# Kernel tuning notes

Measured on AMD Instinct MI355X. Metric: run time of the kernel, lower is better.

## Reference

```python
import jax, jax.numpy as jnp
import numpy as np
from jax import lax

MAX_LENGTH = 10
SOS_TOKEN = 0
B, S, H, V = 64, 128, 1024, 32000


def setup_inputs() -> dict:
    key = jax.random.key(0)
    ks = jax.random.split(key, 16)
    sc = 0.02
    return {
        "encoder_outputs": jax.random.normal(ks[0], (B, S, H), jnp.float32),
        "hidden": jax.random.normal(ks[1], (1, B, H), jnp.float32),
        "target": jax.random.randint(ks[2], (B, MAX_LENGTH), 0, V, jnp.int32),
        "emb_W": jax.random.normal(ks[3], (V, H), jnp.float32) * sc,
        "Wa_w": jax.random.normal(ks[4], (H, H), jnp.float32) * sc,
        "Wa_b": jnp.zeros((H,), jnp.float32),
        "Ua_w": jax.random.normal(ks[5], (H, H), jnp.float32) * sc,
        "Ua_b": jnp.zeros((H,), jnp.float32),
        "Va_w": jax.random.normal(ks[6], (1, H), jnp.float32) * sc,
        "Va_b": jnp.zeros((1,), jnp.float32),
        "W_ih": jax.random.normal(ks[7], (3 * H, 2 * H), jnp.float32) * sc,
        "W_hh": jax.random.normal(ks[8], (3 * H, H), jnp.float32) * sc,
        "b_ih": jnp.zeros((3 * H,), jnp.float32),
        "b_hh": jnp.zeros((3 * H,), jnp.float32),
        "out_W": jax.random.normal(ks[9], (V, H), jnp.float32) * sc,
        "out_b": jnp.zeros((V,), jnp.float32),
    }


def reference(encoder_outputs, hidden, target, emb_W, Wa_w, Wa_b, Ua_w, Ua_b,
              Va_w, Va_b, W_ih, W_hh, b_ih, b_hh, out_W, out_b):
    # teacher-forced decoder input tokens: [SOS, target[:, :T-1]]
    sos = jnp.full((target.shape[0], 1), SOS_TOKEN, target.dtype)
    tokens = jnp.concatenate([sos, target[:, :MAX_LENGTH - 1]], axis=1)  # [B,T]

    # Ua(keys) is constant across steps -> hoist (same math as per-step recompute)
    Uk = jnp.einsum('bsh,gh->bsg', encoder_outputs, Ua_w) + Ua_b  # [B,S,H]

    def step(h, tok):  # h: [B,H], tok: [B]
        emb = emb_W[tok]                                   # [B,H]
        q = h @ Wa_w.T + Wa_b                              # [B,H]
        score = jnp.tanh(q[:, None, :] + Uk) @ Va_w[0] + Va_b[0]  # [B,S]
        w = jax.nn.softmax(score, axis=-1)                 # [B,S]
        ctx = jnp.einsum('bs,bsh->bh', w, encoder_outputs) # [B,H]
        x = jnp.concatenate([emb, ctx], axis=-1)           # [B,2H]
        gi = x @ W_ih.T + b_ih
        gh = h @ W_hh.T + b_hh
        ir, iz, inn = jnp.split(gi, 3, axis=-1)
        hr, hz, hn = jnp.split(gh, 3, axis=-1)
        r = jax.nn.sigmoid(ir + hr)
        z = jax.nn.sigmoid(iz + hz)
        n = jnp.tanh(inn + r * hn)
        h_new = (1.0 - z) * n + z * h
        logits = h_new @ out_W.T + out_b                   # [B,V]
        return h_new, (logits, w)

    hT, (outs, ws) = lax.scan(step, hidden[0], tokens.T)   # outs [T,B,V]
    outputs = jnp.transpose(outs, (1, 0, 2))               # [B,T,V]
    attns = jnp.transpose(ws, (1, 0, 2))                   # [B,T,S]
    return jax.nn.log_softmax(outputs, axis=-1), hT[None], attns
```

## Files before the change

kernel.cpp:

```cpp
#include <hip/hip_runtime.h>

#define B_  64
#define S_  128
#define H_  1024
#define V_  32000
#define T_  10

typedef unsigned short ushort_t;
typedef unsigned int uint32;
typedef __attribute__((ext_vector_type(8))) short bf16x8;
typedef __attribute__((ext_vector_type(4))) float f32x4;

__device__ __forceinline__ ushort_t f2bf(float x) {
    uint32 u = __float_as_uint(x);
    u += 0x7fffu + ((u >> 16) & 1u);
    return (ushort_t)(u >> 16);
}
__device__ __forceinline__ float bf2f(ushort_t h) {
    return __uint_as_float(((uint32)h) << 16);
}
__device__ __forceinline__ uint32 pk2(float a, float b) {
    return (uint32)f2bf(a) | ((uint32)f2bf(b) << 16);
}

typedef const __attribute__((address_space(1))) void gas_void;
typedef __attribute__((address_space(3))) void las_void;
__device__ __forceinline__ void gload_lds16(const ushort_t* g, ushort_t* l) {
    __builtin_amdgcn_global_load_lds((gas_void*)g, (las_void*)l, 16, 0, 0);
}

template<int BM, int BN, int WC, bool SPLIT, bool AF32, int CMODE>
__launch_bounds__(256)
__global__ void gemm_bf(const float* __restrict__ Af,
                        const ushort_t* __restrict__ Ah, const ushort_t* __restrict__ Al,
                        int lda,
                        const ushort_t* __restrict__ Bh, const ushort_t* __restrict__ Bl,
                        int ldb,
                        int K, int kchunk,
                        const float* __restrict__ bias,
                        float* __restrict__ C, int ldc, size_t czstride)
{
    constexpr int WR = 4 / WC;
    constexpr int MF = BM / WR / 16;
    constexpr int NF = BN / WC / 16;
    __shared__ __align__(16) ushort_t lds[(SPLIT ? 2 : 1) * (BM + BN) * 32];
    ushort_t* ldsAh = lds;
    ushort_t* ldsAl = lds + BM * 32;
    ushort_t* ldsBh = lds + (SPLIT ? 2 : 1) * BM * 32;
    ushort_t* ldsBl = ldsBh + BN * 32;

    const int tid  = threadIdx.x;
    const int wid  = tid >> 6;
    const int lane = tid & 63;
    const int lr   = lane & 15;
    const int lk   = lane >> 4;
    const int m0   = blockIdx.y * BM;
    const int n0   = blockIdx.x * BN;
    const int wrow = wid / WC, wcol = wid % WC;
    const int mW   = wrow * (BM / WR);
    const int nW   = wcol * (BN / WC);

    f32x4 acc[MF][NF];
    #pragma unroll
    for (int i = 0; i < MF; i++)
        #pragma unroll
        for (int j = 0; j < NF; j++)
            acc[i][j] = (f32x4){0.f, 0.f, 0.f, 0.f};

    const int kbeg = blockIdx.z * kchunk;
    const int kend = (kbeg + kchunk < K) ? (kbeg + kchunk) : K;

    for (int k0 = kbeg; k0 < kend; k0 += 32) {
        __syncthreads();
        if constexpr (AF32) {
            #pragma unroll
            for (int p = 0; p < BM * 4 / 256; p++) {
                int c = p * 256 + tid, row = c >> 2, slot = c & 3;
                const float* src = Af + (size_t)(m0 + row) * lda + k0 + slot * 8;
                float4 x0 = *(const float4*)src;
                float4 x1 = *(const float4*)(src + 4);
                uint4 hv;
                hv.x = pk2(x0.x, x0.y); hv.y = pk2(x0.z, x0.w);
                hv.z = pk2(x1.x, x1.y); hv.w = pk2(x1.z, x1.w);
                *(uint4*)&ldsAh[row * 32 + slot * 8] = hv;
                if constexpr (SPLIT) {
                    uint4 lv;
                    lv.x = pk2(x0.x - bf2f((ushort_t)(hv.x & 0xffff)), x0.y - bf2f((ushort_t)(hv.x >> 16)));
                    lv.y = pk2(x0.z - bf2f((ushort_t)(hv.y & 0xffff)), x0.w - bf2f((ushort_t)(hv.y >> 16)));
                    lv.z = pk2(x1.x - bf2f((ushort_t)(hv.z & 0xffff)), x1.y - bf2f((ushort_t)(hv.z >> 16)));
                    lv.w = pk2(x1.z - bf2f((ushort_t)(hv.w & 0xffff)), x1.w - bf2f((ushort_t)(hv.w >> 16)));
                    *(uint4*)&ldsAl[row * 32 + slot * 8] = lv;
                }
            }
        } else {
            for (int is = wid; is < BM / 16; is += 4) {
                int row = is * 16 + (lane >> 2), chk = lane & 3;
                size_t off = (size_t)(m0 + row) * lda + k0 + chk * 8;
                gload_lds16(Ah + off, &ldsAh[is * 512]);
                if constexpr (SPLIT) gload_lds16(Al + off, &ldsAl[is * 512]);
            }
        }
        for (int is = wid; is < BN / 16; is += 4) {
            int row = is * 16 + (lane >> 2), chk = lane & 3;
            size_t off = (size_t)(n0 + row) * ldb + k0 + chk * 8;
            gload_lds16(Bh + off, &ldsBh[is * 512]);
            if constexpr (SPLIT) gload_lds16(Bl + off, &ldsBl[is * 512]);
        }
        __syncthreads();
        bf16x8 aH[MF], bH[NF], aL[MF], bL[NF];
        #pragma unroll
        for (int i = 0; i < MF; i++) {
            aH[i] = *(const bf16x8*)&ldsAh[(mW + i * 16 + lr) * 32 + lk * 8];
            if constexpr (SPLIT) aL[i] = *(const bf16x8*)&ldsAl[(mW + i * 16 + lr) * 32 + lk * 8];
        }
        #pragma unroll
        for (int j = 0; j < NF; j++) {
            bH[j] = *(const bf16x8*)&ldsBh[(nW + j * 16 + lr) * 32 + lk * 8];
            if constexpr (SPLIT) bL[j] = *(const bf16x8*)&ldsBl[(nW + j * 16 + lr) * 32 + lk * 8];
        }
        #pragma unroll
        for (int i = 0; i < MF; i++)
            #pragma unroll
            for (int j = 0; j < NF; j++) {
                acc[i][j] = __builtin_amdgcn_mfma_f32_16x16x32_bf16(aH[i], bH[j], acc[i][j], 0, 0, 0);
                if constexpr (SPLIT) {
                    acc[i][j] = __builtin_amdgcn_mfma_f32_16x16x32_bf16(aH[i], bL[j], acc[i][j], 0, 0, 0);
                    acc[i][j] = __builtin_amdgcn_mfma_f32_16x16x32_bf16(aL[i], bH[j], acc[i][j], 0, 0, 0);
                }
            }
    }
    float* Cz = C + (size_t)blockIdx.z * czstride;
    #pragma unroll
    for (int i = 0; i < MF; i++)
        #pragma unroll
        for (int j = 0; j < NF; j++)
            #pragma unroll
            for (int r = 0; r < 4; r++) {
                int gr  = m0 + mW + i * 16 + lk * 4 + r;
                int col = n0 + nW + j * 16 + lr;
                float v = acc[i][j][r];
                if (CMODE == 0) {
                    if (bias) v += bias[col];
                    Cz[(size_t)gr * ldc + col] = v;
                } else {
                    int b = gr & 63, t = gr >> 6;
                    C[((size_t)(b * T_ + t)) * V_ + col] = v + bias[col];
                }
            }
}

__global__ __launch_bounds__(256) void cast_bf16_k(const float* __restrict__ in,
                                                   ushort_t* __restrict__ out, int n8)
{
    int i = blockIdx.x * 256 + threadIdx.x;
    if (i < n8) {
        float4 a = ((const float4*)in)[2 * i];
        float4 b = ((const float4*)in)[2 * i + 1];
        uint4 v;
        v.x = pk2(a.x, a.y); v.y = pk2(a.z, a.w);
        v.z = pk2(b.x, b.y); v.w = pk2(b.z, b.w);
        ((uint4*)out)[i] = v;
    }
}

__global__ __launch_bounds__(256) void cast_hilo_k(const float* __restrict__ in,
                                                   ushort_t* __restrict__ hi,
                                                   ushort_t* __restrict__ lo, int n8)
{
    int i = blockIdx.x * 256 + threadIdx.x;
    if (i < n8) {
        float4 a = ((const float4*)in)[2 * i];
        float4 b = ((const float4*)in)[2 * i + 1];
        uint4 hv, lv;
        hv.x = pk2(a.x, a.y); hv.y = pk2(a.z, a.w);
        hv.z = pk2(b.x, b.y); hv.w = pk2(b.z, b.w);
        lv.x = pk2(a.x - bf2f((ushort_t)(hv.x & 0xffff)), a.y - bf2f((ushort_t)(hv.x >> 16)));
        lv.y = pk2(a.z - bf2f((ushort_t)(hv.y & 0xffff)), a.w - bf2f((ushort_t)(hv.y >> 16)));
        lv.z = pk2(b.x - bf2f((ushort_t)(hv.z & 0xffff)), b.y - bf2f((ushort_t)(hv.z >> 16)));
        lv.w = pk2(b.z - bf2f((ushort_t)(hv.w & 0xffff)), b.w - bf2f((ushort_t)(hv.w >> 16)));
        ((uint4*)hi)[i] = hv;
        ((uint4*)lo)[i] = lv;
    }
}

__global__ __launch_bounds__(256) void gatherhl_k(const int* __restrict__ target,
                                                  const float* __restrict__ emb_W,
                                                  ushort_t* __restrict__ Eh,
                                                  ushort_t* __restrict__ El)
{
    int idx = blockIdx.x * 256 + threadIdx.x;
    int r = idx >> 7, c8 = idx & 127;
    int t = r >> 6, b = r & 63;
    int tok = (t == 0) ? 0 : target[b * T_ + t - 1];
    const float* src = emb_W + (size_t)tok * H_ + c8 * 8;
    float4 a = *(const float4*)src;
    float4 c = *(const float4*)(src + 4);
    uint4 hv, lv;
    hv.x = pk2(a.x, a.y); hv.y = pk2(a.z, a.w);
    hv.z = pk2(c.x, c.y); hv.w = pk2(c.z, c.w);
    lv.x = pk2(a.x - bf2f((ushort_t)(hv.x & 0xffff)), a.y - bf2f((ushort_t)(hv.x >> 16)));
    lv.y = pk2(a.z - bf2f((ushort_t)(hv.y & 0xffff)), a.w - bf2f((ushort_t)(hv.y >> 16)));
    lv.z = pk2(c.x - bf2f((ushort_t)(hv.z & 0xffff)), c.y - bf2f((ushort_t)(hv.z >> 16)));
    lv.w = pk2(c.z - bf2f((ushort_t)(hv.w & 0xffff)), c.w - bf2f((ushort_t)(hv.w >> 16)));
    ((uint4*)(Eh + (size_t)r * H_))[c8] = hv;
    ((uint4*)(El + (size_t)r * H_))[c8] = lv;
}

__global__ __launch_bounds__(256) void score_k(const float* __restrict__ Uk,
                                               const float* __restrict__ qgh_part,
                                               const float* __restrict__ Wa_b,
                                               const float* __restrict__ Va_w,
                                               const float* __restrict__ Va_b,
                                               float* __restrict__ scores)
{
    int s = blockIdx.x, b = blockIdx.y;
    int tid = threadIdx.x;
    float4 qq = ((const float4*)Wa_b)[tid];
    #pragma unroll
    for (int kz = 0; kz < 4; kz++) {
        float4 p = ((const float4*)(qgh_part + (size_t)kz * B_ * 4096 + (size_t)b * 4096))[tid];
        qq.x += p.x; qq.y += p.y; qq.z += p.z; qq.w += p.w;
    }
    float4 u = ((const float4*)(Uk + ((size_t)b * S_ + s) * H_))[tid];
    float4 v = ((const float4*)Va_w)[tid];
    float acc = v.x * tanhf(u.x + qq.x) + v.y * tanhf(u.y + qq.y)
              + v.z * tanhf(u.z + qq.z) + v.w * tanhf(u.w + qq.w);
    for (int off = 32; off > 0; off >>= 1) acc += __shfl_down(acc, off, 64);
    __shared__ float part[4];
    if ((tid & 63) == 0) part[tid >> 6] = acc;
    __syncthreads();
    if (tid == 0) scores[b * S_ + s] = part[0] + part[1] + part[2] + part[3] + Va_b[0];
}

__global__ __launch_bounds__(256) void softctx_k(const float* __restrict__ scores,
                                                 const float* __restrict__ enc,
                                                 ushort_t* __restrict__ ctx_hi,
                                                 ushort_t* __restrict__ ctx_lo,
                                                 float* __restrict__ attn_out, int t)
{
    int hc = blockIdx.x, b = blockIdx.y;
    int tid = threadIdx.x;
    __shared__ float sc[S_], el[S_];
    if (tid < S_) sc[tid] = scores[b * S_ + tid];
    __syncthreads();
    float mx = -1e30f;
    for (int s = 0; s < S_; s++) mx = fmaxf(mx, sc[s]);
    if (tid < S_) el[tid] = expf(sc[tid] - mx);
    __syncthreads();
    float sum = 0.f;
    for (int s = 0; s < S_; s++) sum += el[s];
    float inv = 1.f / sum;
    int h = hc * 256 + tid;
    const float* ep = enc + (size_t)b * S_ * H_ + h;
    float acc = 0.f;
    for (int s = 0; s < S_; s++) acc += el[s] * ep[(size_t)s * H_];
    acc *= inv;
    ushort_t chi = f2bf(acc);
    ctx_hi[(size_t)b * H_ + h] = chi;
    ctx_lo[(size_t)b * H_ + h] = f2bf(acc - bf2f(chi));
    if (hc == 0 && tid < S_) attn_out[((size_t)b * T_ + t) * S_ + tid] = el[tid] * inv;
}

__global__ __launch_bounds__(256) void combine_k(const float* __restrict__ giemb_t,
                                                 const float* __restrict__ gi_part,
                                                 const float* __restrict__ qgh_part,
                                                 const ushort_t* __restrict__ Hh,
                                                 const ushort_t* __restrict__ Hl,
                                                 int t,
                                                 float* __restrict__ out_hidden,
                                                 const float* __restrict__ b_hh)
{
    int i = blockIdx.x * 256 + threadIdx.x;
    int b = i >> 10, g = i & 1023;
    float ir = giemb_t[(size_t)b * 3072 + g];
    float iz = giemb_t[(size_t)b * 3072 + 1024 + g];
    float in = giemb_t[(size_t)b * 3072 + 2048 + g];
    float hr = b_hh[g], hz = b_hh[1024 + g], hn_ = b_hh[2048 + g];
    #pragma unroll
    for (int kz = 0; kz < 4; kz++) {
        const float* gp = gi_part + (size_t)kz * B_ * 3072 + (size_t)b * 3072;
        ir += gp[g]; iz += gp[1024 + g]; in += gp[2048 + g];
        const float* qp = qgh_part + (size_t)kz * B_ * 4096 + (size_t)b * 4096 + 1024;
        hr += qp[g]; hz += qp[1024 + g]; hn_ += qp[2048 + g];
    }
    float h = bf2f(Hh[(size_t)t * B_ * H_ + i]) + bf2f(Hl[(size_t)t * B_ * H_ + i]);
    float r = 1.f / (1.f + expf(-(ir + hr)));
    float z = 1.f / (1.f + expf(-(iz + hz)));
    float n = tanhf(in + r * hn_);
    float hn = (1.f - z) * n + z * h;
    ushort_t hih = f2bf(hn);
    ushort_t* Hhw = (ushort_t*)Hh; ushort_t* Hlw = (ushort_t*)Hl;
    Hhw[(size_t)(t + 1) * B_ * H_ + i] = hih;
    Hlw[(size_t)(t + 1) * B_ * H_ + i] = f2bf(hn - bf2f(hih));
    if (out_hidden) out_hidden[i] = hn;
}

__global__ __launch_bounds__(1024) void lsm_k(float* __restrict__ out)
{
    float4* p = (float4*)(out + (size_t)blockIdx.x * V_);
    int tid = threadIdx.x;
    float mx = -1e30f, sm = 0.f;
    for (int v = tid; v < V_ / 4; v += 1024) {
        float4 x = p[v];
        float xs[4] = {x.x, x.y, x.z, x.w};
        #pragma unroll
        for (int j = 0; j < 4; j++) {
            float m2 = fmaxf(mx, xs[j]);
            sm = sm * expf(mx - m2) + expf(xs[j] - m2);
            mx = m2;
        }
    }
    for (int off = 32; off > 0; off >>= 1) {
        float mo = __shfl_down(mx, off, 64);
        float so = __shfl_down(sm, off, 64);
        float m2 = fmaxf(mx, mo);
        sm = sm * expf(mx - m2) + so * expf(mo - m2);
        mx = m2;
    }
    __shared__ float pm[16], ps[16];
    __shared__ float lse_s;
    if ((tid & 63) == 0) { pm[tid >> 6] = mx; ps[tid >> 6] = sm; }
    __syncthreads();
    if (tid == 0) {
        float m = pm[0], s = ps[0];
        for (int i = 1; i < 16; i++) {
            float m2 = fmaxf(m, pm[i]);
            s = s * expf(m - m2) + ps[i] * expf(pm[i] - m2);
            m = m2;
        }
        lse_s = m + logf(s);
    }
    __syncthreads();
    float lse = lse_s;
    for (int v = tid; v < V_ / 4; v += 1024) {
        float4 x = p[v];
        x.x -= lse; x.y -= lse; x.z -= lse; x.w -= lse;
        p[v] = x;
    }
}

extern "C" void kernel_launch(void* const* d_in, const int* in_sizes, int n_in,
                              void* d_out, int out_size, void* d_ws, size_t ws_size,
                              hipStream_t stream)
{
    (void)in_sizes; (void)n_in; (void)out_size; (void)ws_size;
    const float* enc    = (const float*)d_in[0];
    const float* hidden = (const float*)d_in[1];
    const int*   target = (const int*)d_in[2];
    const float* emb_W  = (const float*)d_in[3];
    const float* Wa_w   = (const float*)d_in[4];
    const float* Wa_b   = (const float*)d_in[5];
    const float* Ua_w   = (const float*)d_in[6];
    const float* Ua_b   = (const float*)d_in[7];
    const float* Va_w   = (const float*)d_in[8];
    const float* Va_b   = (const float*)d_in[9];
    const float* W_ih   = (const float*)d_in[10];
    const float* W_hh   = (const float*)d_in[11];
    const float* b_ih   = (const float*)d_in[12];
    const float* b_hh   = (const float*)d_in[13];
    const float* out_W  = (const float*)d_in[14];
    const float* out_b  = (const float*)d_in[15];

    float* out_logits = (float*)d_out;
    float* out_hidden = out_logits + (size_t)B_ * T_ * V_;
    float* out_attn   = out_hidden + (size_t)B_ * H_;

    char* w = (char*)d_ws;
    auto alloc = [&](size_t bytes) { char* p = w; w += (bytes + 255) & ~(size_t)255; return p; };
    ushort_t* outW_bf = (ushort_t*)alloc((size_t)V_ * H_ * 2);
    float*    Uk      = (float*)alloc((size_t)B_ * S_ * H_ * 4);
    ushort_t* Ua_hi   = (ushort_t*)alloc((size_t)H_ * H_ * 2);
    ushort_t* Ua_lo   = (ushort_t*)alloc((size_t)H_ * H_ * 2);
    ushort_t* Wih_hi  = (ushort_t*)alloc((size_t)3 * H_ * 2 * H_ * 2);
    ushort_t* Wih_lo  = (ushort_t*)alloc((size_t)3 * H_ * 2 * H_ * 2);
    ushort_t* Wc_hi   = (ushort_t*)alloc((size_t)4 * H_ * H_ * 2);
    ushort_t* Wc_lo   = (ushort_t*)alloc((size_t)4 * H_ * H_ * 2);
    ushort_t* E_hi    = (ushort_t*)alloc((size_t)T_ * B_ * H_ * 2);
    ushort_t* E_lo    = (ushort_t*)alloc((size_t)T_ * B_ * H_ * 2);
    ushort_t* H_hi    = (ushort_t*)alloc((size_t)(T_ + 1) * B_ * H_ * 2);
    ushort_t* H_lo    = (ushort_t*)alloc((size_t)(T_ + 1) * B_ * H_ * 2);
    float*    giemb   = (float*)alloc((size_t)T_ * B_ * 3 * H_ * 4);
    float*    gi_part = (float*)alloc((size_t)4 * B_ * 3 * H_ * 4);
    float*    qgh_part= (float*)alloc((size_t)4 * B_ * 4 * H_ * 4);
    ushort_t* ctx_hi  = (ushort_t*)alloc((size_t)B_ * H_ * 2);
    ushort_t* ctx_lo  = (ushort_t*)alloc((size_t)B_ * H_ * 2);
    float*    scores  = (float*)alloc((size_t)B_ * S_ * 4);

    cast_bf16_k<<<V_ * H_ / 8 / 256, 256, 0, stream>>>(out_W, outW_bf, V_ * H_ / 8);
    cast_hilo_k<<<H_ * H_ / 8 / 256, 256, 0, stream>>>(Ua_w, Ua_hi, Ua_lo, H_ * H_ / 8);
    cast_hilo_k<<<3 * H_ * 2 * H_ / 8 / 256, 256, 0, stream>>>(W_ih, Wih_hi, Wih_lo, 3 * H_ * 2 * H_ / 8);
    cast_hilo_k<<<H_ * H_ / 8 / 256, 256, 0, stream>>>(Wa_w, Wc_hi, Wc_lo, H_ * H_ / 8);
    cast_hilo_k<<<3 * H_ * H_ / 8 / 256, 256, 0, stream>>>(W_hh, Wc_hi + (size_t)H_ * H_,
                                                           Wc_lo + (size_t)H_ * H_, 3 * H_ * H_ / 8);
    cast_hilo_k<<<B_ * H_ / 8 / 256, 256, 0, stream>>>(hidden, H_hi, H_lo, B_ * H_ / 8);
    gatherhl_k<<<T_ * B_ * H_ / 8 / 256, 256, 0, stream>>>(target, emb_W, E_hi, E_lo);

    gemm_bf<128, 128, 2, true, true, 0><<<dim3(H_ / 128, B_ * S_ / 128, 1), 256, 0, stream>>>(
        enc, nullptr, nullptr, H_, Ua_hi, Ua_lo, H_, H_, H_, Ua_b, Uk, H_, 0);
    gemm_bf<128, 128, 2, true, false, 0><<<dim3(3 * H_ / 128, T_ * B_ / 128, 1), 256, 0, stream>>>(
        nullptr, E_hi, E_lo, H_, Wih_hi, Wih_lo, 2 * H_, H_, H_, b_ih, giemb, 3 * H_, 0);

    for (int t = 0; t < T_; t++) {
        float* gi_t = giemb + (size_t)t * B_ * 3 * H_;
        const ushort_t* hh = H_hi + (size_t)t * B_ * H_;
        const ushort_t* hl = H_lo + (size_t)t * B_ * H_;
        gemm_bf<64, 64, 4, true, false, 0><<<dim3(4 * H_ / 64, 1, 4), 256, 0, stream>>>(
            nullptr, hh, hl, H_, Wc_hi, Wc_lo, H_, H_, H_ / 4, nullptr,
            qgh_part, 4 * H_, (size_t)B_ * 4 * H_);
        score_k<<<dim3(S_, B_), 256, 0, stream>>>(Uk, qgh_part, Wa_b, Va_w, Va_b, scores);
        softctx_k<<<dim3(H_ / 256, B_), 256, 0, stream>>>(scores, enc, ctx_hi, ctx_lo, out_attn, t);
        gemm_bf<64, 64, 4, true, false, 0><<<dim3(3 * H_ / 64, 1, 4), 256, 0, stream>>>(
            nullptr, ctx_hi, ctx_lo, H_, Wih_hi + H_, Wih_lo + H_, 2 * H_, H_, H_ / 4, nullptr,
            gi_part, 3 * H_, (size_t)B_ * 3 * H_);
        combine_k<<<B_ * H_ / 256, 256, 0, stream>>>(
            gi_t, gi_part, qgh_part, H_hi, H_lo, t,
            (t == T_ - 1) ? out_hidden : nullptr, b_hh);
    }

    gemm_bf<128, 128, 2, false, false, 2><<<dim3(V_ / 128, T_ * B_ / 128, 1), 256, 0, stream>>>(
        nullptr, H_hi + (size_t)B_ * H_, nullptr, H_, outW_bf, nullptr, H_, H_, H_,
        out_b, out_logits, 0, 0);
    lsm_k<<<B_ * T_, 1024, 0, stream>>>(out_logits);
}
```

Baseline: 988.9 us.

## Fuse ctx-GEMM with GRU combine, batch casts, add XCD-aware tile swizzle

Replaces the split-K context GEMM plus separate combine kernel with a single gigru_k that computes the context part of the input gates and applies the GRU update in its epilogue. This removes the gi_part partial buffer and one launch per step. All hi/lo casts, including the encoder outputs, are merged into one grid-stride kernel, so the Uk GEMM now loads pre-split bf16 instead of converting fp32 in its inner loop. An XCD-aware block-index swizzle is added to the large GEMMs to improve L2 locality. The trade-offs are that gigru_k runs only 32 blocks with a full K loop, and the encoder cast adds a pass over memory.

```diff
diff --git a/kernel.cpp b/kernel.cpp
--- a/kernel.cpp
+++ b/kernel.cpp
@@ -29,16 +29,16 @@
     __builtin_amdgcn_global_load_lds((gas_void*)g, (las_void*)l, 16, 0, 0);
 }
 
-template<int BM, int BN, int WC, bool SPLIT, bool AF32, int CMODE>
+template<int BM, int BN, int WC, bool SPLIT, int CMODE, int SWZ>
 __launch_bounds__(256)
-__global__ void gemm_bf(const float* __restrict__ Af,
-                        const ushort_t* __restrict__ Ah, const ushort_t* __restrict__ Al,
+__global__ void gemm_bf(const ushort_t* __restrict__ Ah, const ushort_t* __restrict__ Al,
                         int lda,
                         const ushort_t* __restrict__ Bh, const ushort_t* __restrict__ Bl,
                         int ldb,
                         int K, int kchunk,
                         const float* __restrict__ bias,
-                        float* __restrict__ C, int ldc, size_t czstride)
+                        float* __restrict__ C, int ldc, size_t czstride,
+                        int swz_q, int swz_r)
 {
     constexpr int WR = 4 / WC;
     constexpr int MF = BM / WR / 16;
@@ -54,8 +54,21 @@
     const int lane = tid & 63;
     const int lr   = lane & 15;
     const int lk   = lane >> 4;
-    const int m0   = blockIdx.y * BM;
-    const int n0   = blockIdx.x * BN;
+
+    int m_i, n_i;
+    if (SWZ == 0) {
+        m_i = blockIdx.y; n_i = blockIdx.x;
+    } else {
+        int lin = blockIdx.y * gridDim.x + blockIdx.x;
+        int xcd = lin & 7, idx = lin >> 3;
+        int w = (xcd < swz_r) ? xcd * (swz_q + 1) + idx
+                              : swz_r * (swz_q + 1) + (xcd - swz_r) * swz_q + idx;
+        if (SWZ == 1) { m_i = w / (int)gridDim.x; n_i = w % (int)gridDim.x; }
+        else          { m_i = w % (int)gridDim.y; n_i = w / (int)gridDim.y; }
+    }
+    const int m0 = m_i * BM;
+    const int n0 = n_i * BN;
+
     const int wrow = wid / WC, wcol = wid % WC;
     const int mW   = wrow * (BM / WR);
     const int nW   = wcol * (BN / WC);
@@ -72,33 +85,11 @@
 
     for (int k0 = kbeg; k0 < kend; k0 += 32) {
         __syncthreads();
-        if constexpr (AF32) {
-            #pragma unroll
-            for (int p = 0; p < BM * 4 / 256; p++) {
-                int c = p * 256 + tid, row = c >> 2, slot = c & 3;
-                const float* src = Af + (size_t)(m0 + row) * lda + k0 + slot * 8;
-                float4 x0 = *(const float4*)src;
-                float4 x1 = *(const float4*)(src + 4);
-                uint4 hv;
-                hv.x = pk2(x0.x, x0.y); hv.y = pk2(x0.z, x0.w);
-                hv.z = pk2(x1.x, x1.y); hv.w = pk2(x1.z, x1.w);
-                *(uint4*)&ldsAh[row * 32 + slot * 8] = hv;
-                if constexpr (SPLIT) {
-                    uint4 lv;
-                    lv.x = pk2(x0.x - bf2f((ushort_t)(hv.x & 0xffff)), x0.y - bf2f((ushort_t)(hv.x >> 16)));
-                    lv.y = pk2(x0.z - bf2f((ushort_t)(hv.y & 0xffff)), x0.w - bf2f((ushort_t)(hv.y >> 16)));
-                    lv.z = pk2(x1.x - bf2f((ushort_t)(hv.z & 0xffff)), x1.y - bf2f((ushort_t)(hv.z >> 16)));
-                    lv.w = pk2(x1.z - bf2f((ushort_t)(hv.w & 0xffff)), x1.w - bf2f((ushort_t)(hv.w >> 16)));
-                    *(uint4*)&ldsAl[row * 32 + slot * 8] = lv;
-                }
-            }
-        } else {
-            for (int is = wid; is < BM / 16; is += 4) {
-                int row = is * 16 + (lane >> 2), chk = lane & 3;
-                size_t off = (size_t)(m0 + row) * lda + k0 + chk * 8;
-                gload_lds16(Ah + off, &ldsAh[is * 512]);
-                if constexpr (SPLIT) gload_lds16(Al + off, &ldsAl[is * 512]);
-            }
+        for (int is = wid; is < BM / 16; is += 4) {
+            int row = is * 16 + (lane >> 2), chk = lane & 3;
+            size_t off = (size_t)(m0 + row) * lda + k0 + chk * 8;
+            gload_lds16(Ah + off, &ldsAh[is * 512]);
+            if constexpr (SPLIT) gload_lds16(Al + off, &ldsAl[is * 512]);
         }
         for (int is = wid; is < BN / 16; is += 4) {
             int row = is * 16 + (lane >> 2), chk = lane & 3;
@@ -149,6 +140,108 @@
             }
 }
 
+__launch_bounds__(256)
+__global__ void gigru_k(const ushort_t* __restrict__ ctx_hi, const ushort_t* __restrict__ ctx_lo,
+                        const ushort_t* __restrict__ W2h, const ushort_t* __restrict__ W2l,
+                        const float* __restrict__ giemb_t,
+                        const float* __restrict__ qgh_part,
+                        const float* __restrict__ b_hh,
+                        ushort_t* __restrict__ Hh, ushort_t* __restrict__ Hl,
+                        int t, float* __restrict__ out_hidden)
+{
+    constexpr int BM = 64, BN = 96;
+    __shared__ __align__(16) ushort_t lds[(BM + BN) * 32 * 2];
+    __shared__ float gi_lds[64][97];
+    ushort_t* ldsAh = lds;
+    ushort_t* ldsAl = lds + BM * 32;
+    ushort_t* ldsBh = lds + 2 * BM * 32;
+    ushort_t* ldsBl = ldsBh + BN * 32;
+
+    const int tid = threadIdx.x, wid = tid >> 6, lane = tid & 63;
+    const int lr = lane & 15, lk = lane >> 4;
+    const int g0 = blockIdx.x * 32;
+    const int wr = wid >> 1, wc = wid & 1;
+    const int mW = wr * 32, nW = wc * 48;
+
+    f32x4 acc[2][3];
+    #pragma unroll
+    for (int i = 0; i < 2; i++)
+        #pragma unroll
+        for (int j = 0; j < 3; j++)
+            acc[i][j] = (f32x4){0.f, 0.f, 0.f, 0.f};
+
+    for (int k0 = 0; k0 < H_; k0 += 32) {
+        __syncthreads();
+        {
+            int row = wid * 16 + (lane >> 2);
+            size_t off = (size_t)row * H_ + k0 + (lane & 3) * 8;
+            gload_lds16(ctx_hi + off, &ldsAh[wid * 512]);
+            gload_lds16(ctx_lo + off, &ldsAl[wid * 512]);
+        }
+        for (int is = wid; is < 6; is += 4) {
+            int br = is * 16 + (lane >> 2);
+            int grow = (br >> 5) * H_ + g0 + (br & 31);
+            size_t off = (size_t)grow * (2 * H_) + k0 + (lane & 3) * 8;
+            gload_lds16(W2h + off, &ldsBh[is * 512]);
+            gload_lds16(W2l + off, &ldsBl[is * 512]);
+        }
+        __syncthreads();
+        bf16x8 aH[2], aL[2], bH[3], bL[3];
+        #pragma unroll
+        for (int i = 0; i < 2; i++) {
+            aH[i] = *(const bf16x8*)&ldsAh[(mW + i * 16 + lr) * 32 + lk * 8];
+            aL[i] = *(const bf16x8*)&ldsAl[(mW + i * 16 + lr) * 32 + lk * 8];
+        }
+        #pragma unroll
+        for (int j = 0; j < 3; j++) {
+            bH[j] = *(const bf16x8*)&ldsBh[(nW + j * 16 + lr) * 32 + lk * 8];
+            bL[j] = *(const bf16x8*)&ldsBl[(nW + j * 16 + lr) * 32 + lk * 8];
+        }
+        #pragma unroll
+        for (int i = 0; i < 2; i++)
+            #pragma unroll
+            for (int j = 0; j < 3; j++) {
+                acc[i][j] = __builtin_amdgcn_mfma_f32_16x16x32_bf16(aH[i], bH[j], acc[i][j], 0, 0, 0);
+                acc[i][j] = __builtin_amdgcn_mfma_f32_16x16x32_bf16(aH[i], bL[j], acc[i][j], 0, 0, 0);
+                acc[i][j] = __builtin_amdgcn_mfma_f32_16x16x32_bf16(aL[i], bH[j], acc[i][j], 0, 0, 0);
+            }
+    }
+    __syncthreads();
+    #pragma unroll
+    for (int i = 0; i < 2; i++)
+        #pragma unroll
+        for (int j = 0; j < 3; j++)
+            #pragma unroll
+            for (int r = 0; r < 4; r++)
+                gi_lds[mW + i * 16 + lk * 4 + r][nW + j * 16 + lr] = acc[i][j][r];
+    __syncthreads();
+    #pragma unroll
+    for (int kk = 0; kk < 8; kk++) {
+        int c = kk * 256 + tid;
+        int gl = c & 31, b = c >> 5;
+        int g = g0 + gl;
+        float ir = giemb_t[(size_t)b * 3072 + g]        + gi_lds[b][gl];
+        float iz = giemb_t[(size_t)b * 3072 + 1024 + g] + gi_lds[b][32 + gl];
+        float in = giemb_t[(size_t)b * 3072 + 2048 + g] + gi_lds[b][64 + gl];
+        float hr = b_hh[g], hz = b_hh[1024 + g], hn_ = b_hh[2048 + g];
+        #pragma unroll
+        for (int kz = 0; kz < 4; kz++) {
+            const float* qp = qgh_part + (size_t)kz * B_ * 4096 + (size_t)b * 4096 + 1024;
+            hr += qp[g]; hz += qp[1024 + g]; hn_ += qp[2048 + g];
+        }
+        size_t ih = (size_t)t * B_ * H_ + (size_t)b * H_ + g;
+        float h = bf2f(Hh[ih]) + bf2f(Hl[ih]);
+        float r = 1.f / (1.f + expf(-(ir + hr)));
+        float z = 1.f / (1.f + expf(-(iz + hz)));
+        float n = tanhf(in + r * hn_);
+        float hn = (1.f - z) * n + z * h;
+        ushort_t hih = f2bf(hn);
+        Hh[ih + B_ * H_] = hih;
+        Hl[ih + B_ * H_] = f2bf(hn - bf2f(hih));
+        if (out_hidden) out_hidden[(size_t)b * H_ + g] = hn;
+    }
+}
+
 __global__ __launch_bounds__(256) void cast_bf16_k(const float* __restrict__ in,
                                                    ushort_t* __restrict__ out, int n8)
 {
@@ -163,14 +256,37 @@
     }
 }
 
-__global__ __launch_bounds__(256) void cast_hilo_k(const float* __restrict__ in,
-                                                   ushort_t* __restrict__ hi,
-                                                   ushort_t* __restrict__ lo, int n8)
-{
-    int i = blockIdx.x * 256 + threadIdx.x;
-    if (i < n8) {
-        float4 a = ((const float4*)in)[2 * i];
-        float4 b = ((const float4*)in)[2 * i + 1];
+#define CAN0 1048576
+#define CAN1 131072
+#define CAN2 786432
+#define CAN3 131072
+#define CAN4 393216
+#define CAN5 8192
+#define CAC1 (CAN0)
+#define CAC2 (CAC1+CAN1)
+#define CAC3 (CAC2+CAN2)
+#define CAC4 (CAC3+CAN3)
+#define CAC5 (CAC4+CAN4)
+#define CATOT (CAC5+CAN5)
+__global__ __launch_bounds__(256) void castall_k(const float* __restrict__ s0,
+                                                 const float* __restrict__ s1,
+                                                 const float* __restrict__ s2,
+                                                 const float* __restrict__ s3,
+                                                 const float* __restrict__ s4,
+                                                 const float* __restrict__ s5,
+                                                 ushort_t* __restrict__ hi,
+                                                 ushort_t* __restrict__ lo)
+{
+    for (int i = blockIdx.x * 256 + threadIdx.x; i < CATOT; i += gridDim.x * 256) {
+        const float* s; int j;
+        if      (i < CAC1) { s = s0; j = i; }
+        else if (i < CAC2) { s = s1; j = i - CAC1; }
+        else if (i < CAC3) { s = s2; j = i - CAC2; }
+        else if (i < CAC4) { s = s3; j = i - CAC3; }
+        else if (i < CAC5) { s = s4; j = i - CAC4; }
+        else               { s = s5; j = i - CAC5; }
+        float4 a = ((const float4*)s)[2 * j];
+        float4 b = ((const float4*)s)[2 * j + 1];
         uint4 hv, lv;
         hv.x = pk2(a.x, a.y); hv.y = pk2(a.z, a.w);
         hv.z = pk2(b.x, b.y); hv.w = pk2(b.z, b.w);
@@ -259,40 +375,6 @@
     ctx_hi[(size_t)b * H_ + h] = chi;
     ctx_lo[(size_t)b * H_ + h] = f2bf(acc - bf2f(chi));
     if (hc == 0 && tid < S_) attn_out[((size_t)b * T_ + t) * S_ + tid] = el[tid] * inv;
-}
-
-__global__ __launch_bounds__(256) void combine_k(const float* __restrict__ giemb_t,
-                                                 const float* __restrict__ gi_part,
-                                                 const float* __restrict__ qgh_part,
-                                                 const ushort_t* __restrict__ Hh,
-                                                 const ushort_t* __restrict__ Hl,
-                                                 int t,
-                                                 float* __restrict__ out_hidden,
-                                                 const float* __restrict__ b_hh)
-{
-    int i = blockIdx.x * 256 + threadIdx.x;
-    int b = i >> 10, g = i & 1023;
-    float ir = giemb_t[(size_t)b * 3072 + g];
-    float iz = giemb_t[(size_t)b * 3072 + 1024 + g];
-    float in = giemb_t[(size_t)b * 3072 + 2048 + g];
-    float hr = b_hh[g], hz = b_hh[1024 + g], hn_ = b_hh[2048 + g];
-    #pragma unroll
-    for (int kz = 0; kz < 4; kz++) {
-        const float* gp = gi_part + (size_t)kz * B_ * 3072 + (size_t)b * 3072;
-        ir += gp[g]; iz += gp[1024 + g]; in += gp[2048 + g];
-        const float* qp = qgh_part + (size_t)kz * B_ * 4096 + (size_t)b * 4096 + 1024;
-        hr += qp[g]; hz += qp[1024 + g]; hn_ += qp[2048 + g];
-    }
-    float h = bf2f(Hh[(size_t)t * B_ * H_ + i]) + bf2f(Hl[(size_t)t * B_ * H_ + i]);
-    float r = 1.f / (1.f + expf(-(ir + hr)));
-    float z = 1.f / (1.f + expf(-(iz + hz)));
-    float n = tanhf(in + r * hn_);
-    float hn = (1.f - z) * n + z * h;
-    ushort_t hih = f2bf(hn);
-    ushort_t* Hhw = (ushort_t*)Hh; ushort_t* Hlw = (ushort_t*)Hl;
-    Hhw[(size_t)(t + 1) * B_ * H_ + i] = hih;
-    Hlw[(size_t)(t + 1) * B_ * H_ + i] = f2bf(hn - bf2f(hih));
-    if (out_hidden) out_hidden[i] = hn;
 }
 
 __global__ __launch_bounds__(1024) void lsm_k(float* __restrict__ out)
@@ -367,58 +449,50 @@
 
     char* w = (char*)d_ws;
     auto alloc = [&](size_t bytes) { char* p = w; w += (bytes + 255) & ~(size_t)255; return p; };
+    const size_t HIB_ELEMS = 19922944 + (size_t)(T_ + 1) * B_ * H_;
     ushort_t* outW_bf = (ushort_t*)alloc((size_t)V_ * H_ * 2);
+    ushort_t* HIb     = (ushort_t*)alloc(HIB_ELEMS * 2);
+    ushort_t* LOb     = (ushort_t*)alloc(HIB_ELEMS * 2);
     float*    Uk      = (float*)alloc((size_t)B_ * S_ * H_ * 4);
-    ushort_t* Ua_hi   = (ushort_t*)alloc((size_t)H_ * H_ * 2);
-    ushort_t* Ua_lo   = (ushort_t*)alloc((size_t)H_ * H_ * 2);
-    ushort_t* Wih_hi  = (ushort_t*)alloc((size_t)3 * H_ * 2 * H_ * 2);
-    ushort_t* Wih_lo  = (ushort_t*)alloc((size_t)3 * H_ * 2 * H_ * 2);
-    ushort_t* Wc_hi   = (ushort_t*)alloc((size_t)4 * H_ * H_ * 2);
-    ushort_t* Wc_lo   = (ushort_t*)alloc((size_t)4 * H_ * H_ * 2);
     ushort_t* E_hi    = (ushort_t*)alloc((size_t)T_ * B_ * H_ * 2);
     ushort_t* E_lo    = (ushort_t*)alloc((size_t)T_ * B_ * H_ * 2);
-    ushort_t* H_hi    = (ushort_t*)alloc((size_t)(T_ + 1) * B_ * H_ * 2);
-    ushort_t* H_lo    = (ushort_t*)alloc((size_t)(T_ + 1) * B_ * H_ * 2);
     float*    giemb   = (float*)alloc((size_t)T_ * B_ * 3 * H_ * 4);
-    float*    gi_part = (float*)alloc((size_t)4 * B_ * 3 * H_ * 4);
     float*    qgh_part= (float*)alloc((size_t)4 * B_ * 4 * H_ * 4);
     ushort_t* ctx_hi  = (ushort_t*)alloc((size_t)B_ * H_ * 2);
     ushort_t* ctx_lo  = (ushort_t*)alloc((size_t)B_ * H_ * 2);
     float*    scores  = (float*)alloc((size_t)B_ * S_ * 4);
 
+    ushort_t* enc_hi = HIb;                  ushort_t* enc_lo = LOb;
+    ushort_t* Ua_hi  = HIb + 8388608;        ushort_t* Ua_lo  = LOb + 8388608;
+    ushort_t* Wih_hi = HIb + 9437184;        ushort_t* Wih_lo = LOb + 9437184;
+    ushort_t* Wc_hi  = HIb + 15728640;       ushort_t* Wc_lo  = LOb + 15728640;
+    ushort_t* H_hi   = HIb + 19922944;       ushort_t* H_lo   = LOb + 19922944;
+
     cast_bf16_k<<<V_ * H_ / 8 / 256, 256, 0, stream>>>(out_W, outW_bf, V_ * H_ / 8);
-    cast_hilo_k<<<H_ * H_ / 8 / 256, 256, 0, stream>>>(Ua_w, Ua_hi, Ua_lo, H_ * H_ / 8);
-    cast_hilo_k<<<3 * H_ * 2 * H_ / 8 / 256, 256, 0, stream>>>(W_ih, Wih_hi, Wih_lo, 3 * H_ * 2 * H_ / 8);
-    cast_hilo_k<<<H_ * H_ / 8 / 256, 256, 0, stream>>>(Wa_w, Wc_hi, Wc_lo, H_ * H_ / 8);
-    cast_hilo_k<<<3 * H_ * H_ / 8 / 256, 256, 0, stream>>>(W_hh, Wc_hi + (size_t)H_ * H_,
-                                                           Wc_lo + (size_t)H_ * H_, 3 * H_ * H_ / 8);
-    cast_hilo_k<<<B_ * H_ / 8 / 256, 256, 0, stream>>>(hidden, H_hi, H_lo, B_ * H_ / 8);
+    castall_k<<<2048, 256, 0, stream>>>(enc, Ua_w, W_ih, Wa_w, W_hh, hidden, HIb, LOb);
     gatherhl_k<<<T_ * B_ * H_ / 8 / 256, 256, 0, stream>>>(target, emb_W, E_hi, E_lo);
 
-    gemm_bf<128, 128, 2, true, true, 0><<<dim3(H_ / 128, B_ * S_ / 128, 1), 256, 0, stream>>>(
-        enc, nullptr, nullptr, H_, Ua_hi, Ua_lo, H_, H_, H_, Ua_b, Uk, H_, 0);
-    gemm_bf<128, 128, 2, true, false, 0><<<dim3(3 * H_ / 128, T_ * B_ / 128, 1), 256, 0, stream>>>(
-        nullptr, E_hi, E_lo, H_, Wih_hi, Wih_lo, 2 * H_, H_, H_, b_ih, giemb, 3 * H_, 0);
+    gemm_bf<128, 128, 2, true, 0, 1><<<dim3(8, 64, 1), 256, 0, stream>>>(
+        enc_hi, enc_lo, H_, Ua_hi, Ua_lo, H_, H_, H_, Ua_b, Uk, H_, 0, 64, 0);
+    gemm_bf<128, 128, 2, true, 0, 2><<<dim3(24, 5, 1), 256, 0, stream>>>(
+        E_hi, E_lo, H_, Wih_hi, Wih_lo, 2 * H_, H_, H_, b_ih, giemb, 3 * H_, 0, 15, 0);
 
     for (int t = 0; t < T_; t++) {
         float* gi_t = giemb + (size_t)t * B_ * 3 * H_;
         const ushort_t* hh = H_hi + (size_t)t * B_ * H_;
         const ushort_t* hl = H_lo + (size_t)t * B_ * H_;
-        gemm_bf<64, 64, 4, true, false, 0><<<dim3(4 * H_ / 64, 1, 4), 256, 0, stream>>>(
-            nullptr, hh, hl, H_, Wc_hi, Wc_lo, H_, H_, H_ / 4, nullptr,
-            qgh_part, 4 * H_, (size_t)B_ * 4 * H_);
+        gemm_bf<64, 64, 4, true, 0, 0><<<dim3(4 * H_ / 64, 1, 4), 256, 0, stream>>>(
+            hh, hl, H_, Wc_hi, Wc_lo, H_, H_, H_ / 4, nullptr,
+            qgh_part, 4 * H_, (size_t)B_ * 4 * H_, 0, 0);
         score_k<<<dim3(S_, B_), 256, 0, stream>>>(Uk, qgh_part, Wa_b, Va_w, Va_b, scores);
         softctx_k<<<dim3(H_ / 256, B_), 256, 0, stream>>>(scores, enc, ctx_hi, ctx_lo, out_attn, t);
-        gemm_bf<64, 64, 4, true, false, 0><<<dim3(3 * H_ / 64, 1, 4), 256, 0, stream>>>(
-            nullptr, ctx_hi, ctx_lo, H_, Wih_hi + H_, Wih_lo + H_, 2 * H_, H_, H_ / 4, nullptr,
-            gi_part, 3 * H_, (size_t)B_ * 3 * H_);
-        combine_k<<<B_ * H_ / 256, 256, 0, stream>>>(
-            gi_t, gi_part, qgh_part, H_hi, H_lo, t,
-            (t == T_ - 1) ? out_hidden : nullptr, b_hh);
-    }
-
-    gemm_bf<128, 128, 2, false, false, 2><<<dim3(V_ / 128, T_ * B_ / 128, 1), 256, 0, stream>>>(
-        nullptr, H_hi + (size_t)B_ * H_, nullptr, H_, outW_bf, nullptr, H_, H_, H_,
-        out_b, out_logits, 0, 0);
+        gigru_k<<<H_ / 32, 256, 0, stream>>>(
+            ctx_hi, ctx_lo, Wih_hi + H_, Wih_lo + H_, gi_t, qgh_part, b_hh,
+            H_hi, H_lo, t, (t == T_ - 1) ? out_hidden : nullptr);
+    }
+
+    gemm_bf<128, 128, 2, false, 2, 2><<<dim3(250, 5, 1), 256, 0, stream>>>(
+        H_hi + (size_t)B_ * H_, nullptr, H_, outW_bf, nullptr, H_, H_, H_,
+        out_b, out_logits, 0, 0, 156, 2);
     lsm_k<<<B_ * T_, 1024, 0, stream>>>(out_logits);
 }
```

Measured after the change: 1.152 ms. +16.4%, slower.
